# Optimization experiments

Measured on AMD Instinct MI355X. Metric: run time of the kernel, lower is better.

## Reference

```python
import jax, jax.numpy as jnp
import numpy as np

N_EXPERTS = 8
TOP_K = 2
AUX_COEF = 0.01
Z_COEF = 0.001


def setup_inputs() -> dict:
    key = jax.random.key(0)
    ks = jax.random.split(key, 5)
    B, S, D, F, E = 2, 2048, 768, 2048, N_EXPERTS
    std = 0.02
    std_out = std / np.sqrt(2 * 12)  # scale_init_by_depth, n_layers=12
    return {
        "x": jax.random.normal(ks[0], (B, S, D), jnp.float32),
        "router_w": jax.random.normal(ks[1], (D, E), jnp.float32) * std,
        "w1": jax.random.normal(ks[2], (E, D, F), jnp.float32) * std,
        "w2": jax.random.normal(ks[3], (E, F, D), jnp.float32) * std_out,
        "w3": jax.random.normal(ks[4], (E, D, F), jnp.float32) * std,
    }


def reference(x, router_w, w1, w2, w3):
    B, S, D = x.shape
    E = w1.shape[0]
    x_flat = x.reshape(-1, D)                      # [N, D]
    n_tokens = x_flat.shape[0]

    router_logits = x_flat @ router_w               # [N, E]
    probs = jax.nn.softmax(router_logits.astype(jnp.float32), axis=-1)
    topk_w, topk_i = jax.lax.top_k(probs, TOP_K)    # [N, K]
    topk_w = topk_w / jnp.sum(topk_w, axis=-1, keepdims=True)

    # Combine: equivalent to sort/group dispatch + per-expert GEMM + index_add,
    # expressed as a masked per-expert (fixed, small E) dense pass.
    out = jnp.zeros((n_tokens, D), dtype=x.dtype)
    for e in range(E):
        gate = jnp.sum(jnp.where(topk_i == e, topk_w, 0.0), axis=-1)  # [N] f32
        h = jax.nn.silu(x_flat @ w1[e]) * (x_flat @ w3[e])            # [N, F]
        out = out + gate[:, None].astype(x.dtype) * (h @ w2[e])

    # Switch-style load-balancing aux loss + z-loss
    importance = probs.mean(axis=0)                 # [E]
    top1 = topk_i[:, 0]
    load = jnp.zeros((E,), jnp.float32).at[top1].add(1.0) / n_tokens
    aux_loss = E * jnp.sum(importance * load) * AUX_COEF
    z_loss = jnp.mean(router_logits.astype(jnp.float32) ** 2) * Z_COEF

    return out.reshape(B, S, D), aux_loss, z_loss
```

## Files before the change

kernel.cpp:

```cpp
#include <hip/hip_runtime.h>
#include <hip/hip_bf16.h>

constexpr int NT = 4096;
constexpr int DD = 768;
constexpr int FF = 2048;
constexpr int NE = 8;
constexpr int MAXROWS = 9216;
constexpr int MAXMT128 = 72;

constexpr int IDX_CNTA   = 0;
constexpr int IDX_CNTT1  = 8;
constexpr int IDX_CUR    = 16;
constexpr int IDX_IMP    = 24;
constexpr int IDX_ZSUM   = 32;
constexpr int IDX_NTILES = 33;
constexpr int IDX_OFF    = 34;
constexpr int IDX_EXPT   = 48;

constexpr size_t OFF_META   = 0;
constexpr size_t OFF_TKE    = 1024;
constexpr size_t OFF_GATE   = OFF_TKE    + (size_t)NT*2*4;
constexpr size_t OFF_ROWOF  = OFF_GATE   + (size_t)NT*2*4;
constexpr size_t OFF_TOKROW = OFF_ROWOF  + (size_t)NT*2*4;
constexpr size_t OFF_XG     = 136192;
constexpr size_t OFF_W1T    = OFF_XG  + (size_t)MAXROWS*DD*2;
constexpr size_t OFF_W3T    = OFF_W1T + (size_t)NE*FF*DD*2;
constexpr size_t OFF_W2T    = OFF_W3T + (size_t)NE*FF*DD*2;
constexpr size_t OFF_H      = OFF_W2T + (size_t)NE*FF*DD*2;
constexpr size_t OFF_OP     = OFF_H   + (size_t)MAXROWS*FF*2;

typedef float f32x4 __attribute__((ext_vector_type(4)));
typedef __bf16 bf16x8v __attribute__((ext_vector_type(8)));
typedef unsigned short u16x8 __attribute__((ext_vector_type(8)));

__device__ inline unsigned short f2bf_bits(float f) {
  __bf16 h = (__bf16)f;
  return *(unsigned short*)&h;
}
__device__ inline float bf2f(unsigned short u) {
  unsigned v = (unsigned)u << 16;
  return *(float*)&v;
}

__device__ __forceinline__ void glds16(const void* g, void* l) {
  __builtin_amdgcn_global_load_lds(
      (const __attribute__((address_space(1))) unsigned int*)g,
      (__attribute__((address_space(3))) unsigned int*)l, 16, 0, 0);
}

constexpr int RB = 128;
__global__ __launch_bounds__(256) void router_kernel(const float* __restrict__ x,
    const float* __restrict__ rw, int* __restrict__ meta,
    int* __restrict__ tke, float* __restrict__ gateArr) {
  __shared__ float s_imp[NE];
  __shared__ float s_z;
  __shared__ int s_cnt1[NE], s_cnta[NE];
  if (threadIdx.x < NE) { s_imp[threadIdx.x] = 0.f; s_cnt1[threadIdx.x] = 0; s_cnta[threadIdx.x] = 0; }
  if (threadIdx.x == 0) s_z = 0.f;
  __syncthreads();

  const int wave = threadIdx.x >> 6, lane = threadIdx.x & 63;
  float impacc[NE];
  #pragma unroll
  for (int e = 0; e < NE; ++e) impacc[e] = 0.f;
  float zacc = 0.f;

  for (int t = blockIdx.x * 4 + wave; t < NT; t += RB * 4) {
    float acc[NE];
    #pragma unroll
    for (int e = 0; e < NE; ++e) acc[e] = 0.f;
    const float* xr = x + (size_t)t * DD;
    for (int i = lane; i < DD; i += 64) {
      float xv = xr[i];
      const float* r = rw + i * NE;
      #pragma unroll
      for (int e = 0; e < NE; ++e) acc[e] += xv * r[e];
    }
    #pragma unroll
    for (int off = 32; off > 0; off >>= 1) {
      #pragma unroll
      for (int e = 0; e < NE; ++e) acc[e] += __shfl_xor(acc[e], off);
    }
    float mx = acc[0];
    #pragma unroll
    for (int e = 1; e < NE; ++e) mx = fmaxf(mx, acc[e]);
    float p[NE]; float s = 0.f;
    #pragma unroll
    for (int e = 0; e < NE; ++e) { p[e] = __expf(acc[e] - mx); s += p[e]; }
    float inv = 1.f / s;
    #pragma unroll
    for (int e = 0; e < NE; ++e) p[e] *= inv;
    int e0 = 0; float p0 = p[0];
    #pragma unroll
    for (int e = 1; e < NE; ++e) if (p[e] > p0) { p0 = p[e]; e0 = e; }
    int e1 = -1; float p1 = -1.f;
    #pragma unroll
    for (int e = 0; e < NE; ++e) if (e != e0 && p[e] > p1) { p1 = p[e]; e1 = e; }
    if (lane == 0) {
      #pragma unroll
      for (int e = 0; e < NE; ++e) { impacc[e] += p[e]; zacc += acc[e] * acc[e]; }
      atomicAdd(&s_cnt1[e0], 1);
      atomicAdd(&s_cnta[e0], 1);
      atomicAdd(&s_cnta[e1], 1);
      float gs = 1.f / (p0 + p1);
      tke[t*2]   = e0; tke[t*2+1] = e1;
      gateArr[t*2] = p0 * gs; gateArr[t*2+1] = p1 * gs;
    }
  }
  if (lane == 0) {
    #pragma unroll
    for (int e = 0; e < NE; ++e) atomicAdd(&s_imp[e], impacc[e]);
    atomicAdd(&s_z, zacc);
  }
  __syncthreads();
  float* fmeta = (float*)meta;
  if (threadIdx.x < NE) {
    atomicAdd(&fmeta[IDX_IMP + threadIdx.x], s_imp[threadIdx.x]);
    atomicAdd(&meta[IDX_CNTT1 + threadIdx.x], s_cnt1[threadIdx.x]);
    atomicAdd(&meta[IDX_CNTA + threadIdx.x], s_cnta[threadIdx.x]);
  }
  if (threadIdx.x == NE) atomicAdd(&fmeta[IDX_ZSUM], s_z);
}

__global__ __launch_bounds__(128) void scan_kernel(int* __restrict__ meta,
                                                   float* __restrict__ out_tail) {
  __shared__ int s_off[NE + 1];
  __shared__ int s_nt[NE];
  __shared__ float s_aux;
  const int t = threadIdx.x;
  if (t < NE) s_nt[t] = (meta[IDX_CNTA + t] + 127) >> 7;
  __syncthreads();
  if (t == 0) {
    int off = 0;
    for (int e = 0; e < NE; ++e) { s_off[e] = off; off += s_nt[e]; }
    s_off[NE] = off;
  }
  __syncthreads();
  const int ntiles = s_off[NE];
  if (t < NE) meta[IDX_OFF + t] = s_off[t] << 7;
  if (t == NE) { meta[IDX_OFF + NE] = ntiles << 7; meta[IDX_NTILES] = ntiles; }
  if (t < ntiles) {
    int e = 0;
    while (t >= s_off[e + 1]) e++;
    meta[IDX_EXPT + t] = e;
  }
  float* fmeta = (float*)meta;
  float pl = 0.f;
  if (t < NE)
    pl = (fmeta[IDX_IMP + t] / (float)NT) * ((float)meta[IDX_CNTT1 + t] / (float)NT);
  if (t < 64) {
    #pragma unroll
    for (int off = 4; off > 0; off >>= 1) pl += __shfl_xor(pl, off);
    if (t == 0) s_aux = pl;
  }
  __syncthreads();
  if (t == 0) {
    out_tail[0] = (float)NE * s_aux * 0.01f;
    out_tail[1] = fmeta[IDX_ZSUM] / (float)(NT * NE) * 0.001f;
  }
}

__global__ __launch_bounds__(256) void scatter_kernel(const int* __restrict__ tke,
    int* __restrict__ meta, int* __restrict__ rowof, int* __restrict__ tokrow) {
  __shared__ int s_cnt[NE], s_base[NE];
  const int t = blockIdx.x * 256 + threadIdx.x;
  if (threadIdx.x < NE) s_cnt[threadIdx.x] = 0;
  __syncthreads();
  const int e0 = tke[t*2], e1 = tke[t*2 + 1];
  const int l0 = atomicAdd(&s_cnt[e0], 1);
  const int l1 = atomicAdd(&s_cnt[e1], 1);
  __syncthreads();
  if (threadIdx.x < NE)
    s_base[threadIdx.x] = atomicAdd(&meta[IDX_CUR + threadIdx.x], s_cnt[threadIdx.x]);
  __syncthreads();
  const int r0 = meta[IDX_OFF + e0] + s_base[e0] + l0;
  const int r1 = meta[IDX_OFF + e1] + s_base[e1] + l1;
  rowof[t*2]     = r0;
  rowof[t*2 + 1] = r1;
  tokrow[r0] = t;
  tokrow[r1] = t;
}

__global__ __launch_bounds__(192) void gather_kernel(const float* __restrict__ x,
    const int* __restrict__ tokrow, const int* __restrict__ meta,
    __bf16* __restrict__ Xg) {
  const int row = blockIdx.x;
  if (row >= meta[IDX_OFF + NE]) return;
  const int tok = tokrow[row];
  ushort4* dst = (ushort4*)(Xg + (size_t)row * DD);
  const int i = threadIdx.x;
  ushort4 o;
  if (tok >= 0) {
    float4 v = ((const float4*)(x + (size_t)tok * DD))[i];
    o.x = f2bf_bits(v.x); o.y = f2bf_bits(v.y);
    o.z = f2bf_bits(v.z); o.w = f2bf_bits(v.w);
  } else {
    o.x = o.y = o.z = o.w = 0;
  }
  dst[i] = o;
}

constexpr int TS = 68;
__global__ __launch_bounds__(256) void transpose_cvt_all(
    const float* __restrict__ w1, const float* __restrict__ w3,
    const float* __restrict__ w2, __bf16* __restrict__ W1t,
    __bf16* __restrict__ W3t, __bf16* __restrict__ W2t) {
  const int z = blockIdx.z, which = z >> 3, e = z & 7;
  const float* src; __bf16* dst; int R, C, rt, ct;
  if (which == 0)      { src = w1; dst = W1t; R = DD; C = FF; rt = blockIdx.y; ct = blockIdx.x; }
  else if (which == 1) { src = w3; dst = W3t; R = DD; C = FF; rt = blockIdx.y; ct = blockIdx.x; }
  else                 { src = w2; dst = W2t; R = FF; C = DD; rt = blockIdx.x; ct = blockIdx.y; }
  src += (size_t)e * DD * FF; dst += (size_t)e * DD * FF;
  const int r0 = rt * 64, c0 = ct * 64;
  __shared__ __align__(16) __bf16 tile[64 * TS];
  const int t = threadIdx.x;
  #pragma unroll
  for (int i = 0; i < 4; ++i) {
    int idx = t + i * 256; int r = idx >> 4, q = idx & 15;
    float4 v = *(const float4*)&src[(size_t)(r0 + r) * C + c0 + q * 4];
    ushort4 o;
    o.x = f2bf_bits(v.x); o.y = f2bf_bits(v.y);
    o.z = f2bf_bits(v.z); o.w = f2bf_bits(v.w);
    *(ushort4*)&tile[r * TS + q * 4] = o;
  }
  __syncthreads();
  #pragma unroll
  for (int i = 0; i < 2; ++i) {
    int idx = t + i * 256; int c = idx >> 3, seg = idx & 7;
    u16x8 o;
    #pragma unroll
    for (int k = 0; k < 8; ++k)
      o[k] = *(unsigned short*)&tile[(seg * 8 + k) * TS + c];
    *(u16x8*)&dst[(size_t)(c0 + c) * R + r0 + seg * 8] = o;
  }
}

__global__ __launch_bounds__(256) void gemm1_kernel(const __bf16* __restrict__ Xg,
    const __bf16* __restrict__ W1t, const __bf16* __restrict__ W3t,
    __bf16* __restrict__ Hb, const int* __restrict__ meta) {
  const int mt = blockIdx.y;
  if (mt >= meta[IDX_NTILES]) return;
  const int e = meta[IDX_EXPT + mt];
  const int n0 = blockIdx.x * 64;
  const int m0 = mt * 128;
  __shared__ __align__(16) __bf16 As[128*32], B1s[64*32], B3s[64*32];
  const int t = threadIdx.x, wave = t >> 6, lane = t & 63;
  const __bf16* w1e = W1t + (size_t)e * FF * DD;
  const __bf16* w3e = W3t + (size_t)e * FF * DD;
  const f32x4 zero = {0.f, 0.f, 0.f, 0.f};
  f32x4 acc1[2][4], acc3[2][4];
  #pragma unroll
  for (int i = 0; i < 2; ++i)
    #pragma unroll
    for (int j = 0; j < 4; ++j) { acc1[i][j] = zero; acc3[i][j] = zero; }

  const __bf16* gA  = Xg  + (size_t)(m0 + 32*wave + (lane >> 2)) * DD + (lane & 3) * 8;
  const __bf16* gB1 = w1e + (size_t)(n0 + 16*wave + (lane >> 2)) * DD + (lane & 3) * 8;
  const __bf16* gB3 = w3e + (size_t)(n0 + 16*wave + (lane >> 2)) * DD + (lane & 3) * 8;
  __bf16* lA0 = &As [(32*wave     ) * 32];
  __bf16* lA1 = &As [(32*wave + 16) * 32];
  __bf16* lB1 = &B1s[(16*wave     ) * 32];
  __bf16* lB3 = &B3s[(16*wave     ) * 32];

  for (int k0 = 0; k0 < DD; k0 += 32) {
    glds16(gA  + k0,           lA0);
    glds16(gA  + k0 + 16*DD,   lA1);
    glds16(gB1 + k0,           lB1);
    glds16(gB3 + k0,           lB3);
    __syncthreads();
    bf16x8v a[2], b1[4], b3[4];
    #pragma unroll
    for (int i = 0; i < 2; ++i)
      a[i] = *(const bf16x8v*)&As[(32*wave + 16*i + (lane & 15))*32 + (lane >> 4)*8];
    #pragma unroll
    for (int j = 0; j < 4; ++j) {
      b1[j] = *(const bf16x8v*)&B1s[(16*j + (lane & 15))*32 + (lane >> 4)*8];
      b3[j] = *(const bf16x8v*)&B3s[(16*j + (lane & 15))*32 + (lane >> 4)*8];
    }
    #pragma unroll
    for (int i = 0; i < 2; ++i)
      #pragma unroll
      for (int j = 0; j < 4; ++j) {
        acc1[i][j] = __builtin_amdgcn_mfma_f32_16x16x32_bf16(a[i], b1[j], acc1[i][j], 0, 0, 0);
        acc3[i][j] = __builtin_amdgcn_mfma_f32_16x16x32_bf16(a[i], b3[j], acc3[i][j], 0, 0, 0);
      }
    __syncthreads();
  }
  #pragma unroll
  for (int i = 0; i < 2; ++i) {
    const int rowb = m0 + 32*wave + 16*i + (lane >> 4)*4;
    #pragma unroll
    for (int j = 0; j < 4; ++j) {
      const int col = n0 + 16*j + (lane & 15);
      #pragma unroll
      for (int r = 0; r < 4; ++r) {
        float c1 = acc1[i][j][r], c3 = acc3[i][j][r];
        float h = c1 / (1.f + __expf(-c1)) * c3;
        Hb[(size_t)(rowb + r)*FF + col] = (__bf16)h;
      }
    }
  }
}

__global__ __launch_bounds__(256) void gemm2_kernel(const __bf16* __restrict__ Hb,
    const __bf16* __restrict__ W2t, __bf16* __restrict__ OP,
    const int* __restrict__ meta) {
  const int mt = blockIdx.y;
  if (mt >= meta[IDX_NTILES]) return;
  const int e = meta[IDX_EXPT + mt];
  const int n0 = blockIdx.x * 128;
  const int m0 = mt * 128;
  __shared__ __align__(16) __bf16 As[128*32], Bs[128*32];
  const int t = threadIdx.x, wave = t >> 6, lane = t & 63;
  const int wm = wave & 1, wn = wave >> 1;
  const __bf16* w2e = W2t + (size_t)e * DD * FF;
  const f32x4 zero = {0.f, 0.f, 0.f, 0.f};
  f32x4 acc[4][4];
  #pragma unroll
  for (int i = 0; i < 4; ++i)
    #pragma unroll
    for (int j = 0; j < 4; ++j) acc[i][j] = zero;

  const __bf16* gA = Hb  + (size_t)(m0 + 32*wave + (lane >> 2)) * FF + (lane & 3) * 8;
  const __bf16* gB = w2e + (size_t)(n0 + 32*wave + (lane >> 2)) * FF + (lane & 3) * 8;
  __bf16* lA0 = &As[(32*wave     ) * 32];
  __bf16* lA1 = &As[(32*wave + 16) * 32];
  __bf16* lB0 = &Bs[(32*wave     ) * 32];
  __bf16* lB1 = &Bs[(32*wave + 16) * 32];

  for (int k0 = 0; k0 < FF; k0 += 32) {
    glds16(gA + k0,          lA0);
    glds16(gA + k0 + 16*FF,  lA1);
    glds16(gB + k0,          lB0);
    glds16(gB + k0 + 16*FF,  lB1);
    __syncthreads();
    bf16x8v a[4], b[4];
    #pragma unroll
    for (int i = 0; i < 4; ++i) {
      a[i] = *(const bf16x8v*)&As[(64*wm + 16*i + (lane & 15))*32 + (lane >> 4)*8];
      b[i] = *(const bf16x8v*)&Bs[(64*wn + 16*i + (lane & 15))*32 + (lane >> 4)*8];
    }
    #pragma unroll
    for (int i = 0; i < 4; ++i)
      #pragma unroll
      for (int j = 0; j < 4; ++j)
        acc[i][j] = __builtin_amdgcn_mfma_f32_16x16x32_bf16(a[i], b[j], acc[i][j], 0, 0, 0);
    __syncthreads();
  }
  #pragma unroll
  for (int i = 0; i < 4; ++i) {
    const int rowb = m0 + 64*wm + 16*i + (lane >> 4)*4;
    #pragma unroll
    for (int j = 0; j < 4; ++j) {
      const int col = n0 + 64*wn + 16*j + (lane & 15);
      #pragma unroll
      for (int r = 0; r < 4; ++r)
        OP[(size_t)(rowb + r)*DD + col] = (__bf16)acc[i][j][r];
    }
  }
}

__global__ __launch_bounds__(192) void combine_kernel(const __bf16* __restrict__ OP,
    const int* __restrict__ rowof, const float* __restrict__ gateArr,
    float* __restrict__ out) {
  const int t = blockIdx.x;
  const int r0 = rowof[t*2], r1 = rowof[t*2 + 1];
  const float g0 = gateArr[t*2], g1 = gateArr[t*2 + 1];
  const ushort4* p0 = (const ushort4*)(OP + (size_t)r0 * DD);
  const ushort4* p1 = (const ushort4*)(OP + (size_t)r1 * DD);
  const int i = threadIdx.x;
  ushort4 a = p0[i], b = p1[i];
  float4 o;
  o.x = g0 * bf2f(a.x) + g1 * bf2f(b.x);
  o.y = g0 * bf2f(a.y) + g1 * bf2f(b.y);
  o.z = g0 * bf2f(a.z) + g1 * bf2f(b.z);
  o.w = g0 * bf2f(a.w) + g1 * bf2f(b.w);
  ((float4*)(out + (size_t)t * DD))[i] = o;
}

extern "C" void kernel_launch(void* const* d_in, const int* in_sizes, int n_in,
                              void* d_out, int out_size, void* d_ws, size_t ws_size,
                              hipStream_t stream) {
  const float* x  = (const float*)d_in[0];
  const float* rw = (const float*)d_in[1];
  const float* w1 = (const float*)d_in[2];
  const float* w2 = (const float*)d_in[3];
  const float* w3 = (const float*)d_in[4];
  float* out = (float*)d_out;

  char* ws = (char*)d_ws;
  int*    meta   = (int*)(ws + OFF_META);
  int*    tke    = (int*)(ws + OFF_TKE);
  float*  gateA  = (float*)(ws + OFF_GATE);
  int*    rowof  = (int*)(ws + OFF_ROWOF);
  int*    tokrow = (int*)(ws + OFF_TOKROW);
  __bf16* Xg     = (__bf16*)(ws + OFF_XG);
  __bf16* W1t    = (__bf16*)(ws + OFF_W1T);
  __bf16* W3t    = (__bf16*)(ws + OFF_W3T);
  __bf16* W2t    = (__bf16*)(ws + OFF_W2T);
  __bf16* Hb     = (__bf16*)(ws + OFF_H);
  __bf16* OP     = (__bf16*)(ws + OFF_OP);

  hipMemsetAsync(ws + OFF_META, 0, 1024, stream);
  hipMemsetAsync(ws + OFF_TOKROW, 0xFF, (size_t)MAXROWS * 4, stream);

  transpose_cvt_all<<<dim3(32, 12, 24), 256, 0, stream>>>(w1, w3, w2, W1t, W3t, W2t);

  router_kernel<<<RB, 256, 0, stream>>>(x, rw, meta, tke, gateA);
  scan_kernel<<<1, 128, 0, stream>>>(meta, out + (size_t)NT * DD);
  scatter_kernel<<<NT/256, 256, 0, stream>>>(tke, meta, rowof, tokrow);
  gather_kernel<<<MAXROWS, 192, 0, stream>>>(x, tokrow, meta, Xg);

  gemm1_kernel<<<dim3(FF/64, MAXMT128), 256, 0, stream>>>(Xg, W1t, W3t, Hb, meta);
  gemm2_kernel<<<dim3(DD/128, MAXMT128), 256, 0, stream>>>(Hb, W2t, OP, meta);
  combine_kernel<<<NT, 192, 0, stream>>>(OP, rowof, gateA, out);
}
```

Measured before the change: 378.0 us.

## Enlarge gemm1 tile to 128x128 with 2x2 wave layout; register-only weight transpose

The gate/up GEMM now computes a 128x128 output tile per block, arranged as a 2x2 grid of waves each owning 64x64. The larger tile reuses each loaded A and B fragment across more MFMAs and halves the number of column blocks, which cuts LDS traffic and global loads of Xg. The cost is twice the accumulator registers (two 4x4 arrays), which may lower occupancy or cause spills. Separately, the weight transpose-and-convert kernel drops its LDS tile and transposes 4x4 sub-blocks in registers, writing 8-byte strided stores instead of 16-byte ones.

```diff
diff --git a/kernel.cpp b/kernel.cpp
--- a/kernel.cpp
+++ b/kernel.cpp
@@ -31,7 +31,6 @@
 
 typedef float f32x4 __attribute__((ext_vector_type(4)));
 typedef __bf16 bf16x8v __attribute__((ext_vector_type(8)));
-typedef unsigned short u16x8 __attribute__((ext_vector_type(8)));
 
 __device__ inline unsigned short f2bf_bits(float f) {
   __bf16 h = (__bf16)f;
@@ -200,7 +199,6 @@
   dst[i] = o;
 }
 
-constexpr int TS = 68;
 __global__ __launch_bounds__(256) void transpose_cvt_all(
     const float* __restrict__ w1, const float* __restrict__ w3,
     const float* __restrict__ w2, __bf16* __restrict__ W1t,
@@ -211,27 +209,22 @@
   else if (which == 1) { src = w3; dst = W3t; R = DD; C = FF; rt = blockIdx.y; ct = blockIdx.x; }
   else                 { src = w2; dst = W2t; R = FF; C = DD; rt = blockIdx.x; ct = blockIdx.y; }
   src += (size_t)e * DD * FF; dst += (size_t)e * DD * FF;
-  const int r0 = rt * 64, c0 = ct * 64;
-  __shared__ __align__(16) __bf16 tile[64 * TS];
-  const int t = threadIdx.x;
-  #pragma unroll
-  for (int i = 0; i < 4; ++i) {
-    int idx = t + i * 256; int r = idx >> 4, q = idx & 15;
-    float4 v = *(const float4*)&src[(size_t)(r0 + r) * C + c0 + q * 4];
+  const int sr = threadIdx.x >> 4;
+  const int sc = threadIdx.x & 15;
+  const int r = rt * 64 + 4 * sr, c = ct * 64 + 4 * sc;
+  float4 v[4];
+  #pragma unroll
+  for (int i = 0; i < 4; ++i)
+    v[i] = *(const float4*)&src[(size_t)(r + i) * C + c];
+  const float* vf = (const float*)v;
+  #pragma unroll
+  for (int j = 0; j < 4; ++j) {
     ushort4 o;
-    o.x = f2bf_bits(v.x); o.y = f2bf_bits(v.y);
-    o.z = f2bf_bits(v.z); o.w = f2bf_bits(v.w);
-    *(ushort4*)&tile[r * TS + q * 4] = o;
-  }
-  __syncthreads();
-  #pragma unroll
-  for (int i = 0; i < 2; ++i) {
-    int idx = t + i * 256; int c = idx >> 3, seg = idx & 7;
-    u16x8 o;
-    #pragma unroll
-    for (int k = 0; k < 8; ++k)
-      o[k] = *(unsigned short*)&tile[(seg * 8 + k) * TS + c];
-    *(u16x8*)&dst[(size_t)(c0 + c) * R + r0 + seg * 8] = o;
+    o.x = f2bf_bits(vf[0*4 + j]);
+    o.y = f2bf_bits(vf[1*4 + j]);
+    o.z = f2bf_bits(vf[2*4 + j]);
+    o.w = f2bf_bits(vf[3*4 + j]);
+    *(ushort4*)&dst[(size_t)(c + j) * R + r] = o;
   }
 }
 
@@ -241,44 +234,47 @@
   const int mt = blockIdx.y;
   if (mt >= meta[IDX_NTILES]) return;
   const int e = meta[IDX_EXPT + mt];
-  const int n0 = blockIdx.x * 64;
+  const int n0 = blockIdx.x * 128;
   const int m0 = mt * 128;
-  __shared__ __align__(16) __bf16 As[128*32], B1s[64*32], B3s[64*32];
+  __shared__ __align__(16) __bf16 As[128*32], B1s[128*32], B3s[128*32];
   const int t = threadIdx.x, wave = t >> 6, lane = t & 63;
+  const int wm = wave & 1, wn = wave >> 1;
   const __bf16* w1e = W1t + (size_t)e * FF * DD;
   const __bf16* w3e = W3t + (size_t)e * FF * DD;
   const f32x4 zero = {0.f, 0.f, 0.f, 0.f};
-  f32x4 acc1[2][4], acc3[2][4];
-  #pragma unroll
-  for (int i = 0; i < 2; ++i)
+  f32x4 acc1[4][4], acc3[4][4];
+  #pragma unroll
+  for (int i = 0; i < 4; ++i)
     #pragma unroll
     for (int j = 0; j < 4; ++j) { acc1[i][j] = zero; acc3[i][j] = zero; }
 
   const __bf16* gA  = Xg  + (size_t)(m0 + 32*wave + (lane >> 2)) * DD + (lane & 3) * 8;
-  const __bf16* gB1 = w1e + (size_t)(n0 + 16*wave + (lane >> 2)) * DD + (lane & 3) * 8;
-  const __bf16* gB3 = w3e + (size_t)(n0 + 16*wave + (lane >> 2)) * DD + (lane & 3) * 8;
+  const __bf16* gB1 = w1e + (size_t)(n0 + 32*wave + (lane >> 2)) * DD + (lane & 3) * 8;
+  const __bf16* gB3 = w3e + (size_t)(n0 + 32*wave + (lane >> 2)) * DD + (lane & 3) * 8;
   __bf16* lA0 = &As [(32*wave     ) * 32];
   __bf16* lA1 = &As [(32*wave + 16) * 32];
-  __bf16* lB1 = &B1s[(16*wave     ) * 32];
-  __bf16* lB3 = &B3s[(16*wave     ) * 32];
+  __bf16* lB10 = &B1s[(32*wave     ) * 32];
+  __bf16* lB11 = &B1s[(32*wave + 16) * 32];
+  __bf16* lB30 = &B3s[(32*wave     ) * 32];
+  __bf16* lB31 = &B3s[(32*wave + 16) * 32];
 
   for (int k0 = 0; k0 < DD; k0 += 32) {
-    glds16(gA  + k0,           lA0);
-    glds16(gA  + k0 + 16*DD,   lA1);
-    glds16(gB1 + k0,           lB1);
-    glds16(gB3 + k0,           lB3);
+    glds16(gA  + k0,          lA0);
+    glds16(gA  + k0 + 16*DD,  lA1);
+    glds16(gB1 + k0,          lB10);
+    glds16(gB1 + k0 + 16*DD,  lB11);
+    glds16(gB3 + k0,          lB30);
+    glds16(gB3 + k0 + 16*DD,  lB31);
     __syncthreads();
-    bf16x8v a[2], b1[4], b3[4];
-    #pragma unroll
-    for (int i = 0; i < 2; ++i)
-      a[i] = *(const bf16x8v*)&As[(32*wave + 16*i + (lane & 15))*32 + (lane >> 4)*8];
-    #pragma unroll
-    for (int j = 0; j < 4; ++j) {
-      b1[j] = *(const bf16x8v*)&B1s[(16*j + (lane & 15))*32 + (lane >> 4)*8];
-      b3[j] = *(const bf16x8v*)&B3s[(16*j + (lane & 15))*32 + (lane >> 4)*8];
-    }
-    #pragma unroll
-    for (int i = 0; i < 2; ++i)
+    bf16x8v a[4], b1[4], b3[4];
+    #pragma unroll
+    for (int i = 0; i < 4; ++i) {
+      a[i]  = *(const bf16x8v*)&As [(64*wm + 16*i + (lane & 15))*32 + (lane >> 4)*8];
+      b1[i] = *(const bf16x8v*)&B1s[(64*wn + 16*i + (lane & 15))*32 + (lane >> 4)*8];
+      b3[i] = *(const bf16x8v*)&B3s[(64*wn + 16*i + (lane & 15))*32 + (lane >> 4)*8];
+    }
+    #pragma unroll
+    for (int i = 0; i < 4; ++i)
       #pragma unroll
       for (int j = 0; j < 4; ++j) {
         acc1[i][j] = __builtin_amdgcn_mfma_f32_16x16x32_bf16(a[i], b1[j], acc1[i][j], 0, 0, 0);
@@ -287,11 +283,11 @@
     __syncthreads();
   }
   #pragma unroll
-  for (int i = 0; i < 2; ++i) {
-    const int rowb = m0 + 32*wave + 16*i + (lane >> 4)*4;
+  for (int i = 0; i < 4; ++i) {
+    const int rowb = m0 + 64*wm + 16*i + (lane >> 4)*4;
     #pragma unroll
     for (int j = 0; j < 4; ++j) {
-      const int col = n0 + 16*j + (lane & 15);
+      const int col = n0 + 64*wn + 16*j + (lane & 15);
       #pragma unroll
       for (int r = 0; r < 4; ++r) {
         float c1 = acc1[i][j][r], c3 = acc3[i][j][r];
@@ -411,7 +407,7 @@
   scatter_kernel<<<NT/256, 256, 0, stream>>>(tke, meta, rowof, tokrow);
   gather_kernel<<<MAXROWS, 192, 0, stream>>>(x, tokrow, meta, Xg);
 
-  gemm1_kernel<<<dim3(FF/64, MAXMT128), 256, 0, stream>>>(Xg, W1t, W3t, Hb, meta);
+  gemm1_kernel<<<dim3(FF/128, MAXMT128), 256, 0, stream>>>(Xg, W1t, W3t, Hb, meta);
   gemm2_kernel<<<dim3(DD/128, MAXMT128), 256, 0, stream>>>(Hb, W2t, OP, meta);
   combine_kernel<<<NT, 192, 0, stream>>>(OP, rowof, gateA, out);
 }
```

New measurement: 440.2 us. 16.5% more time.
